# Kernel optimization log

Hardware: AMD Instinct MI355X
Metric: run time of the kernel (lower is better)

Reference implementation:

```python
import jax, jax.numpy as jnp
import numpy as np

TAU = 1.0          # temperature
PAD = -1.0         # padded_value_indicator
MAX_ITER = 50      # sinkhorn iterations
NEG_BIG = -100000000.0


def setup_inputs() -> dict:
    key = jax.random.key(0)
    k1, k2 = jax.random.split(key)
    B, N = 128, 256
    y_pred = jax.random.normal(k1, (B, N), dtype=jnp.float32)
    y_true = jax.random.randint(k2, (B, N), 0, 5, dtype=jnp.int32)
    return {"y_pred": y_pred, "y_true": y_true}


def deterministic_neural_sort(s, tau, mask):
    # s: [B, n, 1], mask: [B, n] bool
    B, n = s.shape[0], s.shape[1]
    mor = mask[:, :, None] | mask[:, None, :]
    mand = mask[:, :, None] & mask[:, None, :]
    s = jnp.where(mask[:, :, None], NEG_BIG, s)
    A_s = jnp.abs(s - jnp.swapaxes(s, 1, 2))            # [B, n, n]
    A_s = jnp.where(mor, 0.0, A_s)
    # B_mat[b,i,j] = sum_k A_s[b,i,k] (matmul with ones outer product)
    B_mat = A_s.sum(axis=2, keepdims=True)              # [B, n, 1], broadcasts over j
    m = mask.sum(axis=1)                                # [B] number of padded items
    j = jnp.arange(n)
    valid = j[None, :] < (n - m)[:, None]
    scaling = jnp.where(
        valid,
        (n - m)[:, None].astype(jnp.float32) + 1.0 - 2.0 * (j[None, :] + 1).astype(jnp.float32),
        0.0,
    )                                                   # [B, n]
    s0 = jnp.where(mask[:, :, None], 0.0, s)
    C = s0 * scaling[:, None, :]                        # [B,n,1]*[B,1,n] outer product
    P_max = jnp.swapaxes(C - B_mat, 1, 2)
    P_max = jnp.where(mor, -jnp.inf, P_max)
    P_max = jnp.where(mand, 1.0, P_max)
    return jax.nn.softmax(P_max / tau, axis=-1)         # [B, n, n]


def sinkhorn_scaling(mat, mask):
    # mat: [B, n, n], mask: [B, n]
    mor = mask[:, None, :] | mask[:, :, None]
    mand = mask[:, None, :] & mask[:, :, None]
    mat = jnp.where(mor, 0.0, mat)
    mat = jnp.where(mand, 1.0, mat)

    def step(m, _):
        m = m / jnp.clip(m.sum(axis=1, keepdims=True), 1e-10, None)
        m = m / jnp.clip(m.sum(axis=2, keepdims=True), 1e-10, None)
        return m, None

    mat, _ = jax.lax.scan(step, mat, None, length=MAX_ITER)
    return jnp.where(mor, 0.0, mat)


def dcg_at_k(y_pred, y_true, k, gain_fn):
    # returns [B, 1]
    mask = y_true == PAD
    yp = jnp.where(mask, -jnp.inf, y_pred)
    yt = jnp.where(mask, 0.0, y_true)
    order = jnp.argsort(-yp, axis=-1)
    sorted_true = jnp.take_along_axis(yt, order, axis=-1)
    n = y_true.shape[1]
    disc = 1.0 / jnp.log2(jnp.arange(n, dtype=jnp.float32) + 2.0)
    cum = jnp.cumsum(gain_fn(sorted_true) * disc, axis=1)[:, :k]
    return cum[:, k - 1 : k]


def reference(y_pred, y_true):
    B, n = y_pred.shape
    yt = y_true.astype(jnp.float32)
    yt = yt.max() - yt + yt.min()            # relevancy flip as in source
    k = n                                    # self.k is None
    mask = yt == PAD

    P_hat = deterministic_neural_sort(y_pred[:, :, None], TAU, mask)  # [B,n,n]
    P_hat = sinkhorn_scaling(P_hat, mask)[None]                        # [1,B,n,n]
    mor = mask[None, :, :, None] | mask[None, :, None, :]
    P_hat = jnp.where(mor, 0.0, P_hat)

    yt_masked = jnp.where(mask, 0.0, yt)
    gains = jnp.power(2.0, yt_masked) - 1.0                            # powered_relevancies
    ground_truth = jnp.einsum('sbij,bj->sbi', P_hat, gains)            # [1,B,n]
    disc = 1.0 / jnp.log2(jnp.arange(n, dtype=jnp.float32) + 2.0)
    discounted_gains = ground_truth * disc

    idcg = dcg_at_k(yt, yt, k, lambda x: jnp.power(2.0, x) - 1.0).T    # [1,B]
    ndcg = discounted_gains[:, :, :k].sum(axis=-1) / (idcg + 1e-10)    # [1,B]
    idcg_mask = idcg == 0.0
    ndcg = jnp.where(idcg_mask, 0.0, ndcg)
    cnt = (~idcg_mask).sum()
    mean_ndcg = ndcg.sum() / jnp.maximum(cnt.astype(jnp.float32) * ndcg.shape[0], 1.0)
    return jnp.where(cnt > 0, -mean_ndcg, 0.0)
```

## Files before the change

### kernel.cpp

```cpp
#include <hip/hip_runtime.h>


#define NN 256
#define ITERS 50

typedef float v2f __attribute__((ext_vector_type(2)));

__device__ __forceinline__ v2f pkfma(v2f a, v2f b, v2f c) {
    return __builtin_elementwise_fma(a, b, c);
}

template<int C>
__device__ __forceinline__ float dppadd(float v) {
    return v + __int_as_float(__builtin_amdgcn_update_dpp(0, __float_as_int(v), C, 0xF, 0xF, true));
}
template<int C>
__device__ __forceinline__ float dppmax(float v) {
    return fmaxf(v, __int_as_float(__builtin_amdgcn_update_dpp(0, __float_as_int(v), C, 0xF, 0xF, true)));
}
__device__ __forceinline__ float swz16(float v) {
    return __int_as_float(__builtin_amdgcn_ds_swizzle(__float_as_int(v), 0x401F));
}
__device__ __forceinline__ float sum16(float v) {
    v = dppadd<0xB1>(v);
    v = dppadd<0x4E>(v);
    v = dppadd<0x141>(v);
    v = dppadd<0x140>(v);
    return v;
}
__device__ __forceinline__ float sum32f(float v) {
    v = sum16(v);
    v += swz16(v);
    return v;
}
__device__ __forceinline__ float max32f(float v) {
    v = dppmax<0xB1>(v);
    v = dppmax<0x4E>(v);
    v = dppmax<0x141>(v);
    v = dppmax<0x140>(v);
    v = fmaxf(v, swz16(v));
    return v;
}

#if __has_builtin(__builtin_amdgcn_permlane16_swap)
#define HAVE_PLS 1
#endif

__device__ __forceinline__ void sum32_pair(float& A, float& B) {
    A = sum16(A);
    B = sum16(B);
#ifdef HAVE_PLS
    auto r1 = __builtin_amdgcn_permlane16_swap(__float_as_uint(A), __float_as_uint(B), false, false);
    float z = __uint_as_float(r1[0]) + __uint_as_float(r1[1]);
    auto r2 = __builtin_amdgcn_permlane16_swap(__float_as_uint(z), __float_as_uint(z), false, false);
    A = __uint_as_float(r2[0]);
    B = __uint_as_float(r2[1]);
#else
    A += swz16(A);
    B += swz16(B);
#endif
}

#define SINK_B_PHASE                                                         \
    {                                                                        \
        float4 A0 = part4[rslot1];                                           \
        float4 A1 = part4[rslot2];                                           \
        v2f s01 = (v2f){A0.x, A0.y} + (v2f){A1.x, A1.y};                     \
        v2f s23 = (v2f){A0.z, A0.w} + (v2f){A1.z, A1.w};                     \
        float Sx = sum16(s01.x);                                             \
        float Sy = sum16(s01.y);                                             \
        float Sz = sum16(s23.x);                                             \
        float Sw = sum16(s23.y);                                             \
        if (sl == 0) {                                                       \
            float4 C = cvec4[cwslot];                                        \
            float4 F;                                                        \
            F.x = C.x * __builtin_amdgcn_rcpf(fmaxf(C.x * Sx, 1e-10f));      \
            F.y = C.y * __builtin_amdgcn_rcpf(fmaxf(C.y * Sy, 1e-10f));      \
            F.z = C.z * __builtin_amdgcn_rcpf(fmaxf(C.z * Sz, 1e-10f));      \
            F.w = C.w * __builtin_amdgcn_rcpf(fmaxf(C.w * Sw, 1e-10f));      \
            cvec4[cwslot] = F;                                               \
        }                                                                    \
    }

#define SINK_CA_PHASE(EXTRA)                                                 \
    {                                                                        \
        float4 ca = cvec4[crslot];                                           \
        float4 cb = cvec4[crslot + 1];                                       \
        v2f cv2[4] = { {ca.x, ca.y}, {ca.z, ca.w}, {cb.x, cb.y}, {cb.z, cb.w} }; \
        float rs[8];                                                         \
        _Pragma("unroll")                                                    \
        for (int a = 0; a < 8; ++a) {                                        \
            v2f acc = m2[a][0] * cv2[0];                                     \
            acc = pkfma(m2[a][1], cv2[1], acc);                              \
            acc = pkfma(m2[a][2], cv2[2], acc);                              \
            acc = pkfma(m2[a][3], cv2[3], acc);                              \
            rs[a] = acc.x + acc.y;                                           \
        }                                                                    \
        sum32_pair(rs[0], rs[1]);                                            \
        sum32_pair(rs[2], rs[3]);                                            \
        sum32_pair(rs[4], rs[5]);                                            \
        sum32_pair(rs[6], rs[7]);                                            \
        _Pragma("unroll")                                                    \
        for (int a = 0; a < 8; ++a) {                                        \
            float T = fmaxf(r[a] * rs[a], 1e-10f);                           \
            r[a] *= __builtin_amdgcn_rcpf(T);                                \
        }                                                                    \
        EXTRA                                                                \
        {                                                                    \
            v2f p2[4];                                                       \
            _Pragma("unroll")                                                \
            for (int bp = 0; bp < 4; ++bp) {                                 \
                v2f rr = r[0];                                               \
                v2f acc = m2[0][bp] * rr;                                    \
                _Pragma("unroll")                                            \
                for (int a = 1; a < 8; ++a) {                                \
                    v2f ra = r[a];                                           \
                    acc = pkfma(m2[a][bp], ra, acc);                         \
                }                                                            \
                p2[bp] = acc;                                                \
            }                                                                \
            part4[wslot]      = make_float4(p2[0].x, p2[0].y, p2[1].x, p2[1].y); \
            part4[wslot + 32] = make_float4(p2[2].x, p2[2].y, p2[3].x, p2[3].y); \
        }                                                                    \
    }

#define SINK_ITER(EXTRA) { __syncthreads(); SINK_B_PHASE; __syncthreads(); SINK_CA_PHASE(EXTRA) }

#define SNAP_EXTRA                                                           \
    {                                                                        \
        _Pragma("unroll")                                                    \
        for (int a = 0; a < 8; ++a) rsnap[a] = r[a];                         \
        if (t < 72) csnap[t] = cvec4[t];                                     \
    }

#define CHECK_EXTRA                                                          \
    {                                                                        \
        bool okc = true;                                                     \
        _Pragma("unroll")                                                    \
        for (int a = 0; a < 8; ++a)                                          \
            okc &= (__float_as_uint(r[a]) == __float_as_uint(rsnap[a]));     \
        if (t < 72) {                                                        \
            float4 Aq = cvec4[t];                                            \
            float4 Bq = csnap[t];                                            \
            okc &= (__float_as_uint(Aq.x) == __float_as_uint(Bq.x));         \
            okc &= (__float_as_uint(Aq.y) == __float_as_uint(Bq.y));         \
            okc &= (__float_as_uint(Aq.z) == __float_as_uint(Bq.z));         \
            okc &= (__float_as_uint(Aq.w) == __float_as_uint(Bq.w));         \
        }                                                                    \
        if (!__all(okc) && l == 0) convFlag[ci & 1] = 0;                     \
        if (t == 0) convFlag[(ci + 1) & 1] = 1;                              \
    }

__global__ __launch_bounds__(1024, 4) void ndcg_main(const float* __restrict__ yp,
                                                     const int* __restrict__ ytr,
                                                     int nbatch,
                                                     float* __restrict__ ndArr,
                                                     float* __restrict__ cntArr,
                                                     int* __restrict__ doneCnt,
                                                     float* __restrict__ out) {
    const int b = blockIdx.x;
    const int t = threadIdx.x;
    const int l = t & 63;
    const int ti = t >> 5;
    const int tj = t & 31;
    const int cq = t >> 4;
    const int sl = t & 15;

    __shared__ float4 part4[32 * 64];
    __shared__ float4 cvec4[72];
    __shared__ float4 csnap[72];
    __shared__ __align__(16) float sarr[NN], bmarr[NN], garr[NN], darr[NN];
    __shared__ float numAcc, idcgAcc;
    __shared__ int hist[64], wmn[16], wmx[16], gmn, gmx;
    __shared__ float redS[16], redC[16];
    __shared__ int lastFlag;
    __shared__ int convFlag[2];

    float* partf = (float*)part4;

    {
        int mn = 0x7fffffff, mx = (int)0x80000000;
        const int4* y4 = (const int4*)ytr;
        const int n4 = nbatch * (NN / 4);
        for (int i = t; i < n4; i += 1024) {
            int4 v = y4[i];
            mn = min(mn, min(min(v.x, v.y), min(v.z, v.w)));
            mx = max(mx, max(max(v.x, v.y), max(v.z, v.w)));
        }
        for (int mo = 1; mo < 64; mo <<= 1) {
            mn = min(mn, __shfl_xor(mn, mo));
            mx = max(mx, __shfl_xor(mx, mo));
        }
        if (l == 0) { wmn[t >> 6] = mn; wmx[t >> 6] = mx; }
    }
    if (t < 64) hist[t] = 0;
    if (t < 72) cvec4[t] = make_float4(1.0f, 1.0f, 1.0f, 1.0f);
    if (t < 2) convFlag[t] = 1;
    if (t == 0) { numAcc = 0.0f; idcgAcc = 0.0f; }
    __syncthreads();
    if (t == 0) {
        int a = wmn[0], c = wmx[0];
        for (int i = 1; i < 16; ++i) { a = min(a, wmn[i]); c = max(c, wmx[i]); }
        gmn = a; gmx = c;
    }
    __syncthreads();
    const int ymin = gmn, ymax = gmx;

    if (t < NN) {
        sarr[t] = yp[b * NN + t];
        int ytv = ymax - ytr[b * NN + t] + ymin;
        garr[t] = exp2f((float)ytv) - 1.0f;
        darr[t] = 1.0f / log2f((float)t + 2.0f);
        atomicAdd(&hist[min(max(ytv - ymin, 0), 63)], 1);
    }
    __syncthreads();

    {
        int j = t & 255, q = t >> 8;
        float sv = sarr[j];
        float acc = 0.0f;
        int k0 = q * 64;
#pragma unroll 8
        for (int k = 0; k < 64; ++k) acc += fabsf(sv - sarr[k0 + k]);
        partf[q * 256 + j] = acc;
    }
    __syncthreads();
    if (t < NN)
        bmarr[t] = partf[t] + partf[256 + t] + partf[512 + t] + partf[768 + t];
    __syncthreads();

    v2f m2[8][4];
    {
        float sj[8], bm8[8];
        *(float4*)&sj[0]  = ((const float4*)sarr)[tj * 2];
        *(float4*)&sj[4]  = ((const float4*)sarr)[tj * 2 + 1];
        *(float4*)&bm8[0] = ((const float4*)bmarr)[tj * 2];
        *(float4*)&bm8[4] = ((const float4*)bmarr)[tj * 2 + 1];
#pragma unroll
        for (int a = 0; a < 8; ++a) {
            float sc = (float)(255 - 2 * (ti * 8 + a));
            float mv[8];
            float mx = -3.0e38f;
#pragma unroll
            for (int bb = 0; bb < 8; ++bb) {
                mv[bb] = sj[bb] * sc - bm8[bb];
                mx = fmaxf(mx, mv[bb]);
            }
            mx = max32f(mx);
            float z = 0.0f;
#pragma unroll
            for (int bb = 0; bb < 8; ++bb) { mv[bb] = expf(mv[bb] - mx); z += mv[bb]; }
            z = sum32f(z);
            float rz = __builtin_amdgcn_rcpf(z);
#pragma unroll
            for (int bb = 0; bb < 8; ++bb) m2[a][bb >> 1][bb & 1] = mv[bb] * rz;
        }
    }

    if (t < NN) {
        float gain_p = 0.0f;
        int off = 0;
        for (int vb = 63; vb >= 0; --vb) {
            int c = hist[vb];
            if (t >= off && t < off + c) gain_p = exp2f((float)(vb + ymin)) - 1.0f;
            off += c;
        }
        float contrib = sum32f(darr[t] * gain_p);
        contrib += __shfl_xor(contrib, 32);
        if (l == 0) atomicAdd(&idcgAcc, contrib);
    }

    float r[8], rsnap[8];
#pragma unroll
    for (int a = 0; a < 8; ++a) { r[a] = 1.0f; rsnap[a] = 0.0f; }

    const int wslot = ti * 64 + ((tj + ti) & 31);
    const int csc = t >> 5;
    const int hh = cq & 1;
    const int rslot1 = sl * 64 + ((csc + sl) & 31) + 32 * hh;
    const int rslot2 = (sl + 16) * 64 + ((csc + sl + 16) & 31) + 32 * hh;
    const int cwslot = cq + (cq >> 3);
    const int crslot = tj * 2 + (tj >> 2);

    {
        v2f p2[4];
#pragma unroll
        for (int bp = 0; bp < 4; ++bp)
            p2[bp] = ((m2[0][bp] + m2[1][bp]) + (m2[2][bp] + m2[3][bp])) +
                     ((m2[4][bp] + m2[5][bp]) + (m2[6][bp] + m2[7][bp]));
        part4[wslot]      = make_float4(p2[0].x, p2[0].y, p2[1].x, p2[1].y);
        part4[wslot + 32] = make_float4(p2[2].x, p2[2].y, p2[3].x, p2[3].y);
    }

    for (int k = 0; k < 12; ++k) SINK_ITER(;)

    bool conv = false;
    int ci = 0;
#pragma unroll 1
    for (int chunk = 0; chunk < 9; ++chunk) {
        SINK_ITER(;)
        SINK_ITER(SNAP_EXTRA)
        SINK_ITER(;)
        SINK_ITER(CHECK_EXTRA)
        __syncthreads();
        conv = (convFlag[ci & 1] != 0);
        ++ci;
        if (conv) break;
    }
    if (!conv) { SINK_ITER(;) SINK_ITER(;) }

    {
        float4 fa = cvec4[crslot];
        float4 fb = cvec4[crslot + 1];
        float4 ga = ((const float4*)garr)[tj * 2];
        float4 gb = ((const float4*)garr)[tj * 2 + 1];
        v2f gv2[4] = { (v2f){fa.x, fa.y} * (v2f){ga.x, ga.y},
                       (v2f){fa.z, fa.w} * (v2f){ga.z, ga.w},
                       (v2f){fb.x, fb.y} * (v2f){gb.x, gb.y},
                       (v2f){fb.z, fb.w} * (v2f){gb.z, gb.w} };
        float q[8];
#pragma unroll
        for (int a = 0; a < 8; ++a) {
            v2f acc = m2[a][0] * gv2[0];
            acc = pkfma(m2[a][1], gv2[1], acc);
            acc = pkfma(m2[a][2], gv2[2], acc);
            acc = pkfma(m2[a][3], gv2[3], acc);
            q[a] = acc.x + acc.y;
        }
        sum32_pair(q[0], q[1]);
        sum32_pair(q[2], q[3]);
        sum32_pair(q[4], q[5]);
        sum32_pair(q[6], q[7]);
        float partial = 0.0f;
#pragma unroll
        for (int a = 0; a < 8; ++a)
            partial = fmaf(darr[ti * 8 + a] * r[a], q[a], partial);
        if (tj == 0) atomicAdd(&numAcc, partial);
    }
    __syncthreads();

    if (t == 0) {
        float idcg = idcgAcc;
        bool ok = (idcg != 0.0f);
        float nd = ok ? numAcc / (idcg + 1e-10f) : 0.0f;
        __hip_atomic_store(&ndArr[b], nd, __ATOMIC_RELAXED, __HIP_MEMORY_SCOPE_AGENT);
        __hip_atomic_store(&cntArr[b], ok ? 1.0f : 0.0f, __ATOMIC_RELAXED, __HIP_MEMORY_SCOPE_AGENT);
        __threadfence();
        int prev = atomicAdd(doneCnt, 1);
        lastFlag = (prev == nbatch - 1) ? 1 : 0;
    }
    __syncthreads();
    if (lastFlag != 0) {
        __threadfence();
        float s = 0.0f, c = 0.0f;
        for (int i = t; i < nbatch; i += 1024) {
            s += __hip_atomic_load(&ndArr[i], __ATOMIC_RELAXED, __HIP_MEMORY_SCOPE_AGENT);
            c += __hip_atomic_load(&cntArr[i], __ATOMIC_RELAXED, __HIP_MEMORY_SCOPE_AGENT);
        }
        for (int mo = 1; mo < 64; mo <<= 1) { s += __shfl_xor(s, mo); c += __shfl_xor(c, mo); }
        if (l == 0) { redS[t >> 6] = s; redC[t >> 6] = c; }
        __syncthreads();
        if (t == 0) {
            float S = 0.0f, C = 0.0f;
            for (int i = 0; i < 16; ++i) { S += redS[i]; C += redC[i]; }
            out[0] = (C > 0.0f) ? -(S / fmaxf(C, 1.0f)) : 0.0f;
        }
    }
}

extern "C" void kernel_launch(void* const* d_in, const int* in_sizes, int n_in,
                              void* d_out, int out_size, void* d_ws, size_t ws_size,
                              hipStream_t stream) {
    const float* y_pred = (const float*)d_in[0];
    const int* y_true = (const int*)d_in[1];
    const int total = in_sizes[0];
    const int B = total / NN;

    int* doneCnt = (int*)d_ws;
    float* ndArr = (float*)d_ws + 64;
    float* cntArr = ndArr + B;

    hipMemsetAsync(doneCnt, 0, sizeof(int), stream);
    ndcg_main<<<B, 1024, 0, stream>>>(y_pred, y_true, B, ndArr, cntArr, doneCnt,
                                      (float*)d_out);
}
```

Baseline: 165.8 us.

## Replace bitwise fixed-point Sinkhorn exit with tolerance-based row/column sum check

The old early exit required an exact bitwise fixed point of the scaling vectors, checked every four iterations after twelve warm-up iterations using a snapshot. The new path checks whether every row and column normalisation sum lies within 2e-5 of one, reusing sums already computed in the iteration, and starts checking after four warm-up iterations. This drops the snapshot buffer and copies and aims to stop the 50-iteration loop much earlier. In exchange, results now deviate slightly from the full 50-iteration reference, within the tolerance. The plain iteration loops are also marked to not unroll, which shrinks the code.

```diff
diff --git a/kernel.cpp b/kernel.cpp
--- a/kernel.cpp
+++ b/kernel.cpp
@@ -3,6 +3,7 @@
 
 #define NN 256
 #define ITERS 50
+#define CONV_EPS 2e-5f
 
 typedef float v2f __attribute__((ext_vector_type(2)));
 
@@ -82,8 +83,7 @@
         }                                                                    \
     }
 
-#define SINK_CA_PHASE(EXTRA)                                                 \
-    {                                                                        \
+#define SINK_CA_CORE                                                         \
         float4 ca = cvec4[crslot];                                           \
         float4 cb = cvec4[crslot + 1];                                       \
         v2f cv2[4] = { {ca.x, ca.y}, {ca.z, ca.w}, {cb.x, cb.y}, {cb.z, cb.w} }; \
@@ -99,13 +99,9 @@
         sum32_pair(rs[0], rs[1]);                                            \
         sum32_pair(rs[2], rs[3]);                                            \
         sum32_pair(rs[4], rs[5]);                                            \
-        sum32_pair(rs[6], rs[7]);                                            \
-        _Pragma("unroll")                                                    \
-        for (int a = 0; a < 8; ++a) {                                        \
-            float T = fmaxf(r[a] * rs[a], 1e-10f);                           \
-            r[a] *= __builtin_amdgcn_rcpf(T);                                \
-        }                                                                    \
-        EXTRA                                                                \
+        sum32_pair(rs[6], rs[7]);
+
+#define SINK_CA_TAIL                                                         \
         {                                                                    \
             v2f p2[4];                                                       \
             _Pragma("unroll")                                                \
@@ -121,34 +117,63 @@
             }                                                                \
             part4[wslot]      = make_float4(p2[0].x, p2[0].y, p2[1].x, p2[1].y); \
             part4[wslot + 32] = make_float4(p2[2].x, p2[2].y, p2[3].x, p2[3].y); \
+        }
+
+#define SINK_ITER_PLAIN                                                      \
+    {                                                                        \
+        __syncthreads();                                                     \
+        SINK_B_PHASE;                                                        \
+        __syncthreads();                                                     \
+        {                                                                    \
+            SINK_CA_CORE                                                     \
+            _Pragma("unroll")                                                \
+            for (int a = 0; a < 8; ++a) {                                    \
+                float T = fmaxf(r[a] * rs[a], 1e-10f);                       \
+                r[a] *= __builtin_amdgcn_rcpf(T);                            \
+            }                                                                \
+            SINK_CA_TAIL                                                     \
         }                                                                    \
     }
 
-#define SINK_ITER(EXTRA) { __syncthreads(); SINK_B_PHASE; __syncthreads(); SINK_CA_PHASE(EXTRA) }
-
-#define SNAP_EXTRA                                                           \
+#define SINK_ITER_CHECK                                                      \
     {                                                                        \
-        _Pragma("unroll")                                                    \
-        for (int a = 0; a < 8; ++a) rsnap[a] = r[a];                         \
-        if (t < 72) csnap[t] = cvec4[t];                                     \
-    }
-
-#define CHECK_EXTRA                                                          \
-    {                                                                        \
-        bool okc = true;                                                     \
-        _Pragma("unroll")                                                    \
-        for (int a = 0; a < 8; ++a)                                          \
-            okc &= (__float_as_uint(r[a]) == __float_as_uint(rsnap[a]));     \
-        if (t < 72) {                                                        \
-            float4 Aq = cvec4[t];                                            \
-            float4 Bq = csnap[t];                                            \
-            okc &= (__float_as_uint(Aq.x) == __float_as_uint(Bq.x));         \
-            okc &= (__float_as_uint(Aq.y) == __float_as_uint(Bq.y));         \
-            okc &= (__float_as_uint(Aq.z) == __float_as_uint(Bq.z));         \
-            okc &= (__float_as_uint(Aq.w) == __float_as_uint(Bq.w));         \
+        __syncthreads();                                                     \
+        bool okc;                                                            \
+        {                                                                    \
+            float4 A0 = part4[rslot1];                                       \
+            float4 A1 = part4[rslot2];                                       \
+            v2f s01 = (v2f){A0.x, A0.y} + (v2f){A1.x, A1.y};                 \
+            v2f s23 = (v2f){A0.z, A0.w} + (v2f){A1.z, A1.w};                 \
+            float Sx = sum16(s01.x);                                         \
+            float Sy = sum16(s01.y);                                         \
+            float Sz = sum16(s23.x);                                         \
+            float Sw = sum16(s23.y);                                         \
+            float4 C = cvec4[cwslot];            \
+            float sx = C.x * Sx, sy = C.y * Sy, sz = C.z * Sz, sw = C.w * Sw; \
+            okc = (fabsf(sx - 1.0f) <= CONV_EPS) & (fabsf(sy - 1.0f) <= CONV_EPS) & \
+                  (fabsf(sz - 1.0f) <= CONV_EPS) & (fabsf(sw - 1.0f) <= CONV_EPS); \
+            if (sl == 0) {                                                   \
+                float4 F;                                                    \
+                F.x = C.x * __builtin_amdgcn_rcpf(fmaxf(sx, 1e-10f));        \
+                F.y = C.y * __builtin_amdgcn_rcpf(fmaxf(sy, 1e-10f));        \
+                F.z = C.z * __builtin_amdgcn_rcpf(fmaxf(sz, 1e-10f));        \
+                F.w = C.w * __builtin_amdgcn_rcpf(fmaxf(sw, 1e-10f));        \
+                cvec4[cwslot] = F;                                           \
+            }                                                                \
         }                                                                    \
-        if (!__all(okc) && l == 0) convFlag[ci & 1] = 0;                     \
-        if (t == 0) convFlag[(ci + 1) & 1] = 1;                              \
+        __syncthreads();                                                     \
+        {                                                                    \
+            SINK_CA_CORE                                                     \
+            _Pragma("unroll")                                                \
+            for (int a = 0; a < 8; ++a) {                                    \
+                float T = fmaxf(r[a] * rs[a], 1e-10f);                       \
+                okc &= (fabsf(T - 1.0f) <= CONV_EPS);                        \
+                r[a] *= __builtin_amdgcn_rcpf(T);                            \
+            }                                                                \
+            if (!__all(okc) && l == 0) convFlag[ci & 1] = 0;                 \
+            if (t == 0) convFlag[(ci + 1) & 1] = 1;                          \
+            SINK_CA_TAIL                                                     \
+        }                                                                    \
     }
 
 __global__ __launch_bounds__(1024, 4) void ndcg_main(const float* __restrict__ yp,
@@ -168,7 +193,6 @@
 
     __shared__ float4 part4[32 * 64];
     __shared__ float4 cvec4[72];
-    __shared__ float4 csnap[72];
     __shared__ __align__(16) float sarr[NN], bmarr[NN], garr[NN], darr[NN];
     __shared__ float numAcc, idcgAcc;
     __shared__ int hist[64], wmn[16], wmx[16], gmn, gmx;
@@ -270,9 +294,9 @@
         if (l == 0) atomicAdd(&idcgAcc, contrib);
     }
 
-    float r[8], rsnap[8];
-#pragma unroll
-    for (int a = 0; a < 8; ++a) { r[a] = 1.0f; rsnap[a] = 0.0f; }
+    float r[8];
+#pragma unroll
+    for (int a = 0; a < 8; ++a) r[a] = 1.0f;
 
     const int wslot = ti * 64 + ((tj + ti) & 31);
     const int csc = t >> 5;
@@ -292,22 +316,25 @@
         part4[wslot + 32] = make_float4(p2[2].x, p2[2].y, p2[3].x, p2[3].y);
     }
 
-    for (int k = 0; k < 12; ++k) SINK_ITER(;)
+#pragma unroll 1
+    for (int k = 0; k < 4; ++k) SINK_ITER_PLAIN
 
     bool conv = false;
     int ci = 0;
 #pragma unroll 1
-    for (int chunk = 0; chunk < 9; ++chunk) {
-        SINK_ITER(;)
-        SINK_ITER(SNAP_EXTRA)
-        SINK_ITER(;)
-        SINK_ITER(CHECK_EXTRA)
+    for (int chunk = 0; chunk < 11; ++chunk) {
+#pragma unroll 1
+        for (int k = 0; k < 3; ++k) SINK_ITER_PLAIN
+        SINK_ITER_CHECK
         __syncthreads();
         conv = (convFlag[ci & 1] != 0);
         ++ci;
         if (conv) break;
     }
-    if (!conv) { SINK_ITER(;) SINK_ITER(;) }
+    if (!conv) {
+#pragma unroll 1
+        for (int k = 0; k < 2; ++k) SINK_ITER_PLAIN
+    }
 
     {
         float4 fa = cvec4[crslot];
```

After: 169.4 us. +2.1%, slower.
